# Optimization experiments

Hardware: AMD Instinct MI355X
Metric: run time of the kernel (lower is better)

## Reference

```python
import jax, jax.numpy as jnp
import numpy as np

B = 64
BAND = 16384
N_OSC = 32
CH = 64
T_IN = 32
N_NOISE_FRAMES = BAND // 4          # 4096
NOISE_STEP = BAND // N_NOISE_FRAMES  # 4 samples per noise frame
NOISE_COEFFS = NOISE_STEP // 2 + 1   # 3 rfft coefficients
N_UP = int(np.log2(N_NOISE_FRAMES) - np.log2(T_IN))  # 7 doubling blocks
LOWEST_FREQ = 20.0 / 11025.0


def _conv1d(x, w, b, pad):
    # x: (B, Cin, T), w: (Cout, Cin, K)
    out = jax.lax.conv_general_dilated(x, w, (1,), [(pad, pad)],
                                       dimension_numbers=('NCH', 'OIH', 'NCH'))
    return out + b[None, :, None]


def _leaky(x):
    return jnp.where(x > 0, x, 0.2 * x)


def _lin_interp(x, size):
    # torch F.interpolate(mode='linear', align_corners=False) along last axis
    n = x.shape[-1]
    coords = (jnp.arange(size, dtype=jnp.float32) + 0.5) * (n / size) - 0.5
    coords = jnp.clip(coords, 0.0, n - 1.0)
    lo = jnp.floor(coords).astype(jnp.int32)
    hi = jnp.minimum(lo + 1, n - 1)
    frac = (coords - lo.astype(jnp.float32)).astype(x.dtype)
    return x[..., lo] * (1.0 - frac) + x[..., hi] * frac


def setup_inputs() -> dict:
    key = jax.random.key(0)
    ks = jax.random.split(key, 16)
    s = 0.1
    return {
        'x': jax.random.normal(ks[0], (B, T_IN, CH), jnp.float32),
        'noise': jax.random.uniform(ks[1], (B, N_NOISE_FRAMES, NOISE_STEP), jnp.float32, -1.0, 1.0),
        'net_w': jax.random.normal(ks[2], (4, CH, CH, 3), jnp.float32) * s,
        'net_b': jax.random.normal(ks[3], (4, CH), jnp.float32) * s,
        'final_w': jax.random.normal(ks[4], (CH, CH, 3), jnp.float32) * s,
        'final_b': jax.random.normal(ks[5], (CH,), jnp.float32) * s,
        'amp_w': jax.random.normal(ks[6], (N_OSC, CH), jnp.float32) * s,
        'amp_b': jax.random.normal(ks[7], (N_OSC,), jnp.float32) * s,
        'freq_w': jax.random.normal(ks[8], (N_OSC, CH), jnp.float32) * s,
        'freq_b': jax.random.normal(ks[9], (N_OSC,), jnp.float32) * s,
        'nz_init_w': jax.random.normal(ks[10], (CH, CH), jnp.float32) * s,
        'nz_init_b': jax.random.normal(ks[11], (CH,), jnp.float32) * s,
        'nz_up_w': jax.random.normal(ks[12], (N_UP, CH, CH, 3), jnp.float32) * s,
        'nz_up_b': jax.random.normal(ks[13], (N_UP, CH), jnp.float32) * s,
        'nz_final_w': jax.random.normal(ks[14], (NOISE_COEFFS, CH), jnp.float32) * s,
        'nz_final_b': jax.random.normal(ks[15], (NOISE_COEFFS,), jnp.float32) * s,
    }


def reference(x, noise, net_w, net_b, final_w, final_b, amp_w, amp_b, freq_w, freq_b,
              nz_init_w, nz_init_b, nz_up_w, nz_up_b, nz_final_w, nz_final_b):
    z = jnp.transpose(x, (0, 2, 1))  # (B, CH, T_IN)
    for i in range(4):
        z = _leaky(_conv1d(z, net_w[i], net_b[i], 1))
    z = _conv1d(z, final_w, final_b, 1)

    # --- OscillatorBank: sigmoid freq (constrained), abs amp, linear upsample,
    # phase accumulation via cumsum, summed sinusoids ---
    amp = jnp.abs(jnp.einsum('bct,oc->bot', z, amp_w) + amp_b[None, :, None])
    freq = jax.nn.sigmoid(jnp.einsum('bct,oc->bot', z, freq_w) + freq_b[None, :, None])
    freq = LOWEST_FREQ + freq * (1.0 - LOWEST_FREQ)
    amp = _lin_interp(amp, BAND)    # (B, N_OSC, BAND)
    freq = _lin_interp(freq, BAND)  # (B, N_OSC, BAND)
    phase = jnp.cumsum(freq * jnp.pi, axis=-1)
    harm = jnp.sum(amp * jnp.sin(phase), axis=1, keepdims=True)  # (B, 1, BAND)

    # 1x1 conv to rfft coeffs, squared, applied per-frame to uniform noise ---
    y = jnp.einsum('bct,oc->bot', z, nz_init_w) + nz_init_b[None, :, None]
    for i in range(N_UP):
        y = jnp.repeat(y, 2, axis=-1)
        y = _leaky(_conv1d(y, nz_up_w[i], nz_up_b[i], 1))
    coeffs = jnp.einsum('bct,oc->bot', y, nz_final_w) + nz_final_b[None, :, None]
    coeffs = coeffs ** 2                      # squared=True, activation=identity
    coeffs = jnp.transpose(coeffs, (0, 2, 1))  # (B, frames, NOISE_COEFFS)
    spec = jnp.fft.rfft(noise, axis=-1, norm='ortho')   # (B, frames, NOISE_COEFFS)
    filt = spec * coeffs.astype(spec.dtype)
    nz = jnp.fft.irfft(filt, n=NOISE_STEP, axis=-1, norm='ortho')  # (B, frames, step)
    nz = nz.reshape(B, 1, BAND)

    return harm + nz
```

## Files before the change

### kernel.cpp

```cpp
#include <hip/hip_runtime.h>
#include <math.h>

#define LOWEST_FREQ_F 0.00181405895691609977f

typedef short bf16x8 __attribute__((ext_vector_type(8)));
typedef float f32x16 __attribute__((ext_vector_type(16)));

__device__ __forceinline__ float lrelu(float x) { return x > 0.f ? x : 0.2f * x; }
__device__ __forceinline__ float sin_rev(float fr) { return __builtin_amdgcn_sinf(fr); }
__device__ __forceinline__ float bf2f(unsigned short u) {
  union { unsigned int i; float f; } x; x.i = ((unsigned int)u) << 16; return x.f;
}
__device__ __forceinline__ unsigned short f2bf(float f) {
  union { float f; unsigned int i; } x; x.f = f;
  unsigned int r = x.i + 0x7FFFu + ((x.i >> 16) & 1u);
  return (unsigned short)(r >> 16);
}
__device__ __forceinline__ unsigned int pack2(float a, float b) {
  return (unsigned int)f2bf(a) | ((unsigned int)f2bf(b) << 16);
}

__global__ __launch_bounds__(256) void prep_kernel(
    const float* __restrict__ net_w, const float* __restrict__ fin_w,
    const float* __restrict__ amp_w, const float* __restrict__ frq_w,
    const float* __restrict__ nzi_w, const float* __restrict__ nzu_w,
    float* __restrict__ wtF4, float* __restrict__ awfwT,
    float* __restrict__ nzT, short* __restrict__ wfold)
{
  int idx = blockIdx.x * 256 + threadIdx.x;
  if (idx < 20480) {
    int l = idx >> 12, r = idx & 4095;
    int ci = r >> 6, co = r & 63;
    const float* src = (l < 4) ? (net_w + l * 12288) : fin_w;
    const float* wb = src + co * 192 + ci * 3;
    float4 v = make_float4(wb[0], wb[1], wb[2], 0.f);
    ((float4*)wtF4)[idx] = v;
  } else if (idx < 24576) {
    int r = idx - 20480;
    int c2 = r >> 7, rem = r & 127, o = rem >> 2, k = rem & 3;
    int c = c2 * 2 + (k >> 1);
    awfwT[r] = (k & 1) ? frq_w[o * 64 + c] : amp_w[o * 64 + c];
  } else if (idx < 28672) {
    int r = idx - 24576; int c = r >> 6, o = r & 63;
    nzT[r] = nzi_w[o * 64 + c];
  } else if (idx < 28672 + 114688) {
    int r = idx - 28672;
    int l = r >> 14, q = r & 16383;
    int pd = q >> 12, co = (q >> 6) & 63, ci = q & 63;
    const float* wb = nzu_w + l * 12288 + co * 192 + ci * 3;
    float v;
    if      (pd == 0) v = wb[0];
    else if (pd == 1) v = wb[1] + wb[2];
    else if (pd == 2) v = wb[0] + wb[1];
    else              v = wb[2];
    wfold[r] = (short)f2bf(v);
  }
}

template<int TIN>
__device__ __forceinline__ void noise_layer(
    const short* tin, short* tout, const short* __restrict__ wf,
    const float* __restrict__ bias, int tid)
{
  const int L  = tid & 63;
  const int w  = tid >> 6;
  const int mt = w & 1;
  const int ng = w >> 1;

  bf16x8 Af[4][4];
  {
    const short* wb = wf + (mt*32 + (L & 31))*64 + ((L >> 5) << 3);
    #pragma unroll
    for (int pd = 0; pd < 4; ++pd)
      #pragma unroll
      for (int ks = 0; ks < 4; ++ks)
        Af[pd][ks] = *(const bf16x8*)(wb + pd*4096 + ks*16);
  }
  f32x16 binit;
  #pragma unroll
  for (int r = 0; r < 16; ++r)
    binit[r] = bias[mt*32 + (r & 3) + 8*(r >> 2) + 4*(L >> 5)];

  if (tid < 64) { tout[tid] = 0; tout[(2*TIN + 1)*72 + tid] = 0; }

  constexpr int TOT = TIN / 32;
  constexpr int NPG = (TOT + 3) / 4;
  #pragma unroll
  for (int nt = 0; nt < NPG; ++nt) {
    int ntile = ng*NPG + nt;
    if (ntile < TOT) {
      int s = ntile*32 + (L & 31);
      const short* bp = tin + s*72 + ((L >> 5) << 3);
      f32x16 Ce = binit, Co = binit;
      #pragma unroll
      for (int ks = 0; ks < 4; ++ks) {
        bf16x8 Bm = *(const bf16x8*)(bp + ks*16);
        bf16x8 B0 = *(const bf16x8*)(bp + 72 + ks*16);
        bf16x8 Bp = *(const bf16x8*)(bp + 144 + ks*16);
        Ce = __builtin_amdgcn_mfma_f32_32x32x16_bf16(Af[0][ks], Bm, Ce, 0, 0, 0);
        Ce = __builtin_amdgcn_mfma_f32_32x32x16_bf16(Af[1][ks], B0, Ce, 0, 0, 0);
        Co = __builtin_amdgcn_mfma_f32_32x32x16_bf16(Af[2][ks], B0, Co, 0, 0, 0);
        Co = __builtin_amdgcn_mfma_f32_32x32x16_bf16(Af[3][ks], Bp, Co, 0, 0, 0);
      }
      #pragma unroll
      for (int q4 = 0; q4 < 4; ++q4) {
        int co0 = mt*32 + 8*q4 + 4*(L >> 5);
        uint2 ve, vo;
        ve.x = pack2(lrelu(Ce[4*q4+0]), lrelu(Ce[4*q4+1]));
        ve.y = pack2(lrelu(Ce[4*q4+2]), lrelu(Ce[4*q4+3]));
        vo.x = pack2(lrelu(Co[4*q4+0]), lrelu(Co[4*q4+1]));
        vo.y = pack2(lrelu(Co[4*q4+2]), lrelu(Co[4*q4+3]));
        *(uint2*)&tout[(2*s + 1)*72 + co0] = ve;
        *(uint2*)&tout[(2*s + 2)*72 + co0] = vo;
      }
    }
  }
  __syncthreads();
}

__global__ __launch_bounds__(512) void z_front(
    const float* __restrict__ x, const float* __restrict__ wtF4,
    const float* __restrict__ net_b, const float* __restrict__ fin_b,
    const float* __restrict__ awfwT, const float* __restrict__ amp_b,
    const float* __restrict__ frq_b,
    const float* __restrict__ nzT, const float* __restrict__ nzi_b,
    const short* __restrict__ wfold, const float* __restrict__ nzu_b,
    unsigned short* __restrict__ y3, float* __restrict__ amp_o,
    float* __restrict__ frq_o, float* __restrict__ ph_o)
{
  __shared__ __align__(16) char arena[86976];
  short* tileB = (short*)arena;
  short* tileA = (short*)(arena + 37152);
  float* za    = (float*)(arena + 55872);
  float* zb    = (float*)(arena + 65088);
  float* zt    = (float*)(arena + 74304);
  float* fl    = (float*)(arena + 82752);

  const int b   = blockIdx.x;
  const int tid = threadIdx.x;
  const int co  = tid & 63;
  const int wv  = tid >> 6;

  for (int idx = tid; idx < 2048; idx += 512) {
    int t = idx >> 6, c = idx & 63;
    za[c*36 + t + 1] = x[b*2048 + idx];
  }
  if (tid < 64) {
    za[tid*36] = 0.f; za[tid*36 + 33] = 0.f;
    zb[tid*36] = 0.f; zb[tid*36 + 33] = 0.f;
  }
  __syncthreads();

  float* pa = za;
  float* pb = zb;
  for (int l = 0; l < 5; ++l) {
    if (tid < 256) {
      const int q = tid >> 6;
      float bv = (l < 4) ? net_b[l*64 + co] : fin_b[co];
      float acc[8];
      #pragma unroll
      for (int j = 0; j < 8; ++j) acc[j] = bv;

      const float4* wp = ((const float4*)wtF4) + l*4096 + co;
      float4 wA[4], wB[4];
      #pragma unroll
      for (int k = 0; k < 4; ++k) wA[k] = wp[k*64];

      #pragma unroll 2
      for (int cc = 0; cc < 8; ++cc) {
        #pragma unroll
        for (int k = 0; k < 4; ++k) wB[k] = wp[(cc*8 + 4 + k)*64];
        #pragma unroll
        for (int k = 0; k < 4; ++k) {
          const int ci = cc*8 + k;
          const float* rowp = pa + ci*36 + (q << 3);
          float4 zA = *(const float4*)(rowp);
          float4 zB = *(const float4*)(rowp + 4);
          float2 zC = *(const float2*)(rowp + 8);
          float rr[10] = {zA.x, zA.y, zA.z, zA.w, zB.x, zB.y, zB.z, zB.w,
                          zC.x, zC.y};
          float4 wgt = wA[k];
          #pragma unroll
          for (int j = 0; j < 8; ++j) {
            acc[j] = fmaf(wgt.x, rr[j],   acc[j]);
            acc[j] = fmaf(wgt.y, rr[j+1], acc[j]);
            acc[j] = fmaf(wgt.z, rr[j+2], acc[j]);
          }
        }
        if (cc < 7) {
          #pragma unroll
          for (int k = 0; k < 4; ++k) wA[k] = wp[((cc+1)*8 + k)*64];
        }
        #pragma unroll
        for (int k = 0; k < 4; ++k) {
          const int ci = cc*8 + 4 + k;
          const float* rowp = pa + ci*36 + (q << 3);
          float4 zA = *(const float4*)(rowp);
          float4 zB = *(const float4*)(rowp + 4);
          float2 zC = *(const float2*)(rowp + 8);
          float rr[10] = {zA.x, zA.y, zA.z, zA.w, zB.x, zB.y, zB.z, zB.w,
                          zC.x, zC.y};
          float4 wgt = wB[k];
          #pragma unroll
          for (int j = 0; j < 8; ++j) {
            acc[j] = fmaf(wgt.x, rr[j],   acc[j]);
            acc[j] = fmaf(wgt.y, rr[j+1], acc[j]);
            acc[j] = fmaf(wgt.z, rr[j+2], acc[j]);
          }
        }
      }

      if (l < 4) {
        #pragma unroll
        for (int j = 0; j < 8; ++j)
          pb[co*36 + (q << 3) + j + 1] = lrelu(acc[j]);
      } else {
        #pragma unroll
        for (int j = 0; j < 8; ++j) {
          int t = (q << 3) + j;
          pb[co*36 + t] = acc[j];
          zt[t*66 + co] = acc[j];
        }
      }
    }
    __syncthreads();
    float* tp = pa; pa = pb; pb = tp;
  }
  const float* zf = pa;

  {
    const int q = wv;
    float bv0 = nzi_b[co];
    float acc[4];
    #pragma unroll
    for (int j = 0; j < 4; ++j) acc[j] = bv0;
    #pragma unroll 8
    for (int c = 0; c < 64; ++c) {
      float4 zv = *(const float4*)(zf + c*36 + (q << 2));
      float wvv = nzT[c*64 + co];
      acc[0] = fmaf(wvv, zv.x, acc[0]);
      acc[1] = fmaf(wvv, zv.y, acc[1]);
      acc[2] = fmaf(wvv, zv.z, acc[2]);
      acc[3] = fmaf(wvv, zv.w, acc[3]);
    }
    #pragma unroll
    for (int j = 0; j < 4; ++j)
      tileA[((q << 2) + j + 1)*72 + co] = (short)f2bf(acc[j]);
  }
  if (tid < 64) { tileA[tid] = 0; tileA[33*72 + tid] = 0; }

  #pragma unroll
  for (int tt = 0; tt < 2; ++tt) {
    int task = tid + 512*tt;
    int o = task & 31, t = task >> 5;
    float aa = amp_b[o], ff = frq_b[o];
    #pragma unroll 8
    for (int c2 = 0; c2 < 32; ++c2) {
      float4 w4 = ((const float4*)awfwT)[c2*32 + o];
      float2 zv = *(const float2*)(zt + t*66 + c2*2);
      aa = fmaf(w4.x, zv.x, aa); ff = fmaf(w4.y, zv.x, ff);
      aa = fmaf(w4.z, zv.y, aa); ff = fmaf(w4.w, zv.y, ff);
    }
    aa = fabsf(aa);
    float sg = 1.f / (1.f + expf(-ff));
    float fq = LOWEST_FREQ_F + sg * (1.f - LOWEST_FREQ_F);
    amp_o[b*1024 + o*32 + t] = aa;
    frq_o[b*1024 + o*32 + t] = fq;
    fl[o*33 + t] = fq;
  }
  __syncthreads();

  if (wv == 7 && (tid & 63) < 32) {
    const int o = tid & 31;
    double P = 256.0 * (double)fl[o*33];
    double hd = P * 0.5;
    ph_o[b*1024 + o*32] = (float)(hd - floor(hd));
    for (int i = 1; i < 32; ++i) {
      P += 256.0 * ((double)fl[o*33 + i - 1] + (double)fl[o*33 + i]);
      hd = P * 0.5;
      ph_o[b*1024 + o*32 + i] = (float)(hd - floor(hd));
    }
  }

  noise_layer<32> (tileA, tileB, wfold + 0*16384, nzu_b + 0*64, tid);
  noise_layer<64> (tileB, tileA, wfold + 1*16384, nzu_b + 1*64, tid);
  noise_layer<128>(tileA, tileB, wfold + 2*16384, nzu_b + 2*64, tid);

  unsigned short* yb = y3 + (size_t)b * 16384;
  for (int c = tid; c < 2048; c += 512) {
    int row = c >> 3, pos = (c & 7) << 3;
    *(bf16x8*)(yb + c*8) = *(const bf16x8*)&tileB[(row + 1)*72 + pos];
  }
}

template<int STILE>
__global__ __launch_bounds__(256) void mfma_up_t(
    const unsigned short* __restrict__ in, unsigned short* __restrict__ out,
    const short* __restrict__ wf, const float* __restrict__ bias, int Tin)
{
  constexpr int ROWS = STILE + 2;
  constexpr int G    = STILE / 64;
  __shared__ __align__(16) short lB[ROWS * 72];

  const int b   = blockIdx.y;
  const int s0  = blockIdx.x * STILE;
  const int tid = threadIdx.x;
  const int L   = tid & 63;
  const int w   = tid >> 6;
  const int mt  = w & 1;
  const int ng  = w >> 1;

  bf16x8 Af[4][4];
  {
    const short* wb = wf + (mt*32 + (L & 31))*64 + ((L >> 5) << 3);
    #pragma unroll
    for (int pd = 0; pd < 4; ++pd)
      #pragma unroll
      for (int ks = 0; ks < 4; ++ks)
        Af[pd][ks] = *(const bf16x8*)(wb + pd*4096 + ks*16);
  }

  const unsigned short* inb = in + (size_t)b * Tin * 64;
  for (int c = tid; c < ROWS*8; c += 256) {
    int row = c >> 3, pos = (c & 7) << 3;
    int g = s0 - 1 + row;
    bf16x8 v = {0,0,0,0,0,0,0,0};
    if (g >= 0 && g < Tin) v = *(const bf16x8*)(inb + (size_t)g*64 + pos);
    *(bf16x8*)&lB[row*72 + pos] = v;
  }

  f32x16 binit;
  #pragma unroll
  for (int r = 0; r < 16; ++r)
    binit[r] = bias[mt*32 + (r & 3) + 8*(r >> 2) + 4*(L >> 5)];

  __syncthreads();

  unsigned short* outb = out + (size_t)b * (2*Tin) * 64;
  #pragma unroll
  for (int nt = 0; nt < G; ++nt) {
    int s_loc = ng*(32*G) + nt*32 + (L & 31);
    const short* bp = lB + s_loc*72 + ((L >> 5) << 3);
    f32x16 Ce = binit, Co = binit;
    #pragma unroll
    for (int ks = 0; ks < 4; ++ks) {
      bf16x8 Bm = *(const bf16x8*)(bp + ks*16);
      bf16x8 B0 = *(const bf16x8*)(bp + 72 + ks*16);
      bf16x8 Bp = *(const bf16x8*)(bp + 144 + ks*16);
      Ce = __builtin_amdgcn_mfma_f32_32x32x16_bf16(Af[0][ks], Bm, Ce, 0, 0, 0);
      Ce = __builtin_amdgcn_mfma_f32_32x32x16_bf16(Af[1][ks], B0, Ce, 0, 0, 0);
      Co = __builtin_amdgcn_mfma_f32_32x32x16_bf16(Af[2][ks], B0, Co, 0, 0, 0);
      Co = __builtin_amdgcn_mfma_f32_32x32x16_bf16(Af[3][ks], Bp, Co, 0, 0, 0);
    }
    int t0 = (s0 + s_loc) * 2;
    #pragma unroll
    for (int q4 = 0; q4 < 4; ++q4) {
      int co0 = mt*32 + 8*q4 + 4*(L >> 5);
      uint2 ve, vo;
      ve.x = pack2(lrelu(Ce[4*q4+0]), lrelu(Ce[4*q4+1]));
      ve.y = pack2(lrelu(Ce[4*q4+2]), lrelu(Ce[4*q4+3]));
      vo.x = pack2(lrelu(Co[4*q4+0]), lrelu(Co[4*q4+1]));
      vo.y = pack2(lrelu(Co[4*q4+2]), lrelu(Co[4*q4+3]));
      *(uint2*)(outb + (size_t)t0*64 + co0)     = ve;
      *(uint2*)(outb + (size_t)(t0+1)*64 + co0) = vo;
    }
  }
}

__global__ __launch_bounds__(256) void final_fused(
    const unsigned short* __restrict__ in,
    const short* __restrict__ wf, const float* __restrict__ bias,
    const float* __restrict__ nzf_w, const float* __restrict__ nzf_b,
    const float* __restrict__ noise,
    const float* __restrict__ amp, const float* __restrict__ frq,
    const float* __restrict__ ph, float* __restrict__ out)
{
  constexpr int STILE = 128, Tin = 2048, ROWS = STILE + 2, G = STILE / 64;
  __shared__ __align__(16) short lB[ROWS * 72];
  __shared__ __align__(16) short yT[256 * 72];
  __shared__ float al[1024], fqv[1024], pl[1024];
  __shared__ float wl[192];

  const int b   = blockIdx.y;
  const int s0  = blockIdx.x * STILE;
  const int tid = threadIdx.x;
  const int L   = tid & 63;
  const int w   = tid >> 6;
  const int mt  = w & 1;
  const int ng  = w >> 1;

  for (int i = tid; i < 1024; i += 256) {
    al[i]  = amp[b*1024 + i];
    fqv[i] = frq[b*1024 + i];
    pl[i]  = ph[b*1024 + i];
  }
  if (tid < 192) { int o = tid >> 6, c = tid & 63; wl[c*3 + o] = nzf_w[tid]; }

  bf16x8 Af[4][4];
  {
    const short* wb = wf + (mt*32 + (L & 31))*64 + ((L >> 5) << 3);
    #pragma unroll
    for (int pd = 0; pd < 4; ++pd)
      #pragma unroll
      for (int ks = 0; ks < 4; ++ks)
        Af[pd][ks] = *(const bf16x8*)(wb + pd*4096 + ks*16);
  }

  const unsigned short* inb = in + (size_t)b * Tin * 64;
  for (int c = tid; c < ROWS*8; c += 256) {
    int row = c >> 3, pos = (c & 7) << 3;
    int g = s0 - 1 + row;
    bf16x8 v = {0,0,0,0,0,0,0,0};
    if (g >= 0 && g < Tin) v = *(const bf16x8*)(inb + (size_t)g*64 + pos);
    *(bf16x8*)&lB[row*72 + pos] = v;
  }

  f32x16 binit;
  #pragma unroll
  for (int r = 0; r < 16; ++r)
    binit[r] = bias[mt*32 + (r & 3) + 8*(r >> 2) + 4*(L >> 5)];

  __syncthreads();

  #pragma unroll
  for (int nt = 0; nt < G; ++nt) {
    int s_loc = ng*(32*G) + nt*32 + (L & 31);
    const short* bp = lB + s_loc*72 + ((L >> 5) << 3);
    f32x16 Ce = binit, Co = binit;
    #pragma unroll
    for (int ks = 0; ks < 4; ++ks) {
      bf16x8 Bm = *(const bf16x8*)(bp + ks*16);
      bf16x8 B0 = *(const bf16x8*)(bp + 72 + ks*16);
      bf16x8 Bp = *(const bf16x8*)(bp + 144 + ks*16);
      Ce = __builtin_amdgcn_mfma_f32_32x32x16_bf16(Af[0][ks], Bm, Ce, 0, 0, 0);
      Ce = __builtin_amdgcn_mfma_f32_32x32x16_bf16(Af[1][ks], B0, Ce, 0, 0, 0);
      Co = __builtin_amdgcn_mfma_f32_32x32x16_bf16(Af[2][ks], B0, Co, 0, 0, 0);
      Co = __builtin_amdgcn_mfma_f32_32x32x16_bf16(Af[3][ks], Bp, Co, 0, 0, 0);
    }
    #pragma unroll
    for (int q4 = 0; q4 < 4; ++q4) {
      int co0 = mt*32 + 8*q4 + 4*(L >> 5);
      uint2 ve, vo;
      ve.x = pack2(lrelu(Ce[4*q4+0]), lrelu(Ce[4*q4+1]));
      ve.y = pack2(lrelu(Ce[4*q4+2]), lrelu(Ce[4*q4+3]));
      vo.x = pack2(lrelu(Co[4*q4+0]), lrelu(Co[4*q4+1]));
      vo.y = pack2(lrelu(Co[4*q4+2]), lrelu(Co[4*q4+3]));
      *(uint2*)&yT[(2*s_loc)*72 + co0]     = ve;
      *(uint2*)&yT[(2*s_loc + 1)*72 + co0] = vo;
    }
  }
  __syncthreads();

  {
    const short* yr = &yT[tid * 72];
    float c0 = nzf_b[0], c1 = nzf_b[1], c2 = nzf_b[2];
    #pragma unroll
    for (int c8 = 0; c8 < 8; ++c8) {
      bf16x8 v = *(const bf16x8*)(yr + c8*8);
      #pragma unroll
      for (int j = 0; j < 8; ++j) {
        float yv = bf2f((unsigned short)v[j]);
        int c = c8*8 + j;
        c0 = fmaf(wl[c*3+0], yv, c0);
        c1 = fmaf(wl[c*3+1], yv, c1);
        c2 = fmaf(wl[c*3+2], yv, c2);
      }
    }
    c0 *= c0; c1 *= c1; c2 *= c2;

    const int fb = 2*s0 + tid;
    const float4 n = *(const float4*)(noise + ((size_t)b*4096 + fb)*4);
    float F0  = c0 * (n.x + n.y + n.z + n.w) * 0.5f;
    float F1r = c1 * (n.x - n.z) * 0.5f;
    float F1i = -(c1 * (n.y - n.w) * 0.5f);
    float F2  = c2 * (n.x - n.y + n.z - n.w) * 0.5f;
    float r0 = 0.5f * (F0 + 2.f*F1r + F2);
    float r1 = 0.5f * (F0 - 2.f*F1i - F2);
    float r2 = 0.5f * (F0 - 2.f*F1r + F2);
    float r3 = 0.5f * (F0 + 2.f*F1i - F2);

    const int t0 = fb * 4;
    float s0a = 0.f, s1a = 0.f, s2a = 0.f, s3a = 0.f;
    if (t0 < 256) {
      const float tp = (float)(t0 + 1) * 0.5f;
      #pragma unroll 4
      for (int o = 0; o < 32; ++o) {
        float f0 = fqv[o*32], am = al[o*32];
        float hf = 0.5f * f0;
        float v0 = tp * f0, v1 = v0 + hf, v2 = v1 + hf, v3 = v2 + hf;
        s0a += am * sin_rev(v0 - floorf(v0));
        s1a += am * sin_rev(v1 - floorf(v1));
        s2a += am * sin_rev(v2 - floorf(v2));
        s3a += am * sin_rev(v3 - floorf(v3));
      }
    } else if (t0 >= 16128) {
      const float tp = (float)(t0 - 16127) * 0.5f;
      #pragma unroll 4
      for (int o = 0; o < 32; ++o) {
        float f0 = fqv[o*32 + 31], am = al[o*32 + 31], p = pl[o*32 + 31];
        float hf = 0.5f * f0;
        float v0 = p + tp * f0, v1 = v0 + hf, v2 = v1 + hf, v3 = v2 + hf;
        s0a += am * sin_rev(v0 - floorf(v0));
        s1a += am * sin_rev(v1 - floorf(v1));
        s2a += am * sin_rev(v2 - floorf(v2));
        s3a += am * sin_rev(v3 - floorf(v3));
      }
    } else {
      const int i  = (t0 - 256) >> 9;
      const int m0 = (t0 - 256) & 511;
      float mm[4], fa[4], mq[4];
      #pragma unroll
      for (int js = 0; js < 4; ++js) {
        float mmv = (float)(m0 + 1 + js);
        mm[js] = mmv;
        fa[js] = ((float)(m0 + js) + 0.5f) * (1.f/512.f);
        mq[js] = mmv * mmv * (1.f/1024.f);
      }
      #pragma unroll 4
      for (int o = 0; o < 32; ++o) {
        float f0 = fqv[o*32 + i], f1 = fqv[o*32 + i + 1];
        float a0 = al[o*32 + i],  a1 = al[o*32 + i + 1];
        float p  = pl[o*32 + i];
        float df = f1 - f0, da = a1 - a0;
        #pragma unroll
        for (int js = 0; js < 4; ++js) {
          float av   = fmaf(da, fa[js], a0);
          float part = fmaf(df, mq[js], mm[js] * f0);
          float v    = fmaf(part, 0.5f, p);
          float fr   = v - floorf(v);
          float sv   = av * sin_rev(fr);
          if      (js == 0) s0a += sv;
          else if (js == 1) s1a += sv;
          else if (js == 2) s2a += sv;
          else              s3a += sv;
        }
      }
    }
    float4 res = make_float4(s0a + r0, s1a + r1, s2a + r2, s3a + r3);
    *(float4*)(out + ((size_t)b*4096 + fb)*4) = res;
  }
}

extern "C" void kernel_launch(void* const* d_in, const int* in_sizes, int n_in,
                              void* d_out, int out_size, void* d_ws, size_t ws_size,
                              hipStream_t stream) {
  (void)in_sizes; (void)n_in; (void)out_size; (void)ws_size;
  const float* x     = (const float*)d_in[0];
  const float* noise = (const float*)d_in[1];
  const float* net_w = (const float*)d_in[2];
  const float* net_b = (const float*)d_in[3];
  const float* fin_w = (const float*)d_in[4];
  const float* fin_b = (const float*)d_in[5];
  const float* amp_w = (const float*)d_in[6];
  const float* amp_b = (const float*)d_in[7];
  const float* frq_w = (const float*)d_in[8];
  const float* frq_b = (const float*)d_in[9];
  const float* nzi_w = (const float*)d_in[10];
  const float* nzi_b = (const float*)d_in[11];
  const float* nzu_w = (const float*)d_in[12];
  const float* nzu_b = (const float*)d_in[13];
  const float* nzf_w = (const float*)d_in[14];
  const float* nzf_b = (const float*)d_in[15];
  float* out = (float*)d_out;

  short* y3    = (short*)d_ws;
  short* y4    = y3 + (size_t)64*256*64;
  short* y5    = y4 + (size_t)64*512*64;
  short* y6    = y5 + (size_t)64*1024*64;
  short* wfold = y6 + (size_t)64*2048*64;
  float* wtF4  = (float*)(wfold + 7*16384);
  float* awfwT = wtF4 + 81920;
  float* nzT   = awfwT + 4096;
  float* ampv  = nzT + 4096;
  float* frqv  = ampv + 65536;
  float* phv   = frqv + 65536;

  prep_kernel<<<dim3(560), dim3(256), 0, stream>>>(
      net_w, fin_w, amp_w, frq_w, nzi_w, nzu_w, wtF4, awfwT, nzT, wfold);

  z_front<<<dim3(64), dim3(512), 0, stream>>>(
      x, wtF4, net_b, fin_b, awfwT, amp_b, frq_b, nzT, nzi_b,
      wfold, nzu_b, (unsigned short*)y3, ampv, frqv, phv);

  mfma_up_t<64> <<<dim3(4, 64), dim3(256), 0, stream>>>(
      (unsigned short*)y3, (unsigned short*)y4, wfold + 3*16384, nzu_b + 3*64, 256);
  mfma_up_t<128><<<dim3(4, 64), dim3(256), 0, stream>>>(
      (unsigned short*)y4, (unsigned short*)y5, wfold + 4*16384, nzu_b + 4*64, 512);
  mfma_up_t<128><<<dim3(8, 64), dim3(256), 0, stream>>>(
      (unsigned short*)y5, (unsigned short*)y6, wfold + 5*16384, nzu_b + 5*64, 1024);

  final_fused<<<dim3(16, 64), dim3(256), 0, stream>>>(
      (unsigned short*)y6, wfold + 6*16384, nzu_b + 6*64,
      nzf_w, nzf_b, noise, ampv, frqv, phv, out);
}
```

Measured before the change: 210.9 us.

## Fuse three noise upsample layers into one kernel with halo recompute

```diff
diff --git a/kernel.cpp b/kernel.cpp
--- a/kernel.cpp
+++ b/kernel.cpp
@@ -118,6 +118,113 @@
   __syncthreads();
 }
 
+template<int NT, int ROFF, bool TOGLOBAL>
+__device__ __forceinline__ void up_stage(
+    const short* bin, short* bout, unsigned short* gout,
+    const short* __restrict__ wf, const float* __restrict__ bias, int tid)
+{
+  const int L  = tid & 63;
+  const int w  = tid >> 6;
+  const int mt = w & 1;
+  const int pg = w >> 1;
+
+  bf16x8 Af[4][4];
+  {
+    const short* wb = wf + (mt*32 + (L & 31))*64 + ((L >> 5) << 3);
+    #pragma unroll
+    for (int pd = 0; pd < 4; ++pd)
+      #pragma unroll
+      for (int ks = 0; ks < 4; ++ks)
+        Af[pd][ks] = *(const bf16x8*)(wb + pd*4096 + ks*16);
+  }
+  f32x16 binit;
+  #pragma unroll
+  for (int r = 0; r < 16; ++r)
+    binit[r] = bias[mt*32 + (r & 3) + 8*(r >> 2) + 4*(L >> 5)];
+
+  for (int n = pg; n < NT; n += 2) {
+    int sl = n*32 + (L & 31);
+    const short* bp = bin + (sl + ROFF)*72 + ((L >> 5) << 3);
+    f32x16 Ce = binit, Co = binit;
+    #pragma unroll
+    for (int ks = 0; ks < 4; ++ks) {
+      bf16x8 Bm = *(const bf16x8*)(bp + ks*16);
+      bf16x8 B0 = *(const bf16x8*)(bp + 72 + ks*16);
+      bf16x8 Bp = *(const bf16x8*)(bp + 144 + ks*16);
+      Ce = __builtin_amdgcn_mfma_f32_32x32x16_bf16(Af[0][ks], Bm, Ce, 0, 0, 0);
+      Ce = __builtin_amdgcn_mfma_f32_32x32x16_bf16(Af[1][ks], B0, Ce, 0, 0, 0);
+      Co = __builtin_amdgcn_mfma_f32_32x32x16_bf16(Af[2][ks], B0, Co, 0, 0, 0);
+      Co = __builtin_amdgcn_mfma_f32_32x32x16_bf16(Af[3][ks], Bp, Co, 0, 0, 0);
+    }
+    #pragma unroll
+    for (int q4 = 0; q4 < 4; ++q4) {
+      int co0 = mt*32 + 8*q4 + 4*(L >> 5);
+      uint2 ve, vo;
+      ve.x = pack2(lrelu(Ce[4*q4+0]), lrelu(Ce[4*q4+1]));
+      ve.y = pack2(lrelu(Ce[4*q4+2]), lrelu(Ce[4*q4+3]));
+      vo.x = pack2(lrelu(Co[4*q4+0]), lrelu(Co[4*q4+1]));
+      vo.y = pack2(lrelu(Co[4*q4+2]), lrelu(Co[4*q4+3]));
+      if (TOGLOBAL) {
+        *(uint2*)(gout + (size_t)(2*sl)*64 + co0)     = ve;
+        *(uint2*)(gout + (size_t)(2*sl + 1)*64 + co0) = vo;
+      } else {
+        *(uint2*)&bout[(2*sl)*72 + co0]     = ve;
+        *(uint2*)&bout[(2*sl + 1)*72 + co0] = vo;
+      }
+    }
+  }
+}
+
+__global__ __launch_bounds__(256) void up345(
+    const unsigned short* __restrict__ y3, unsigned short* __restrict__ y6,
+    const short* __restrict__ wfold, const float* __restrict__ nzu_b)
+{
+  __shared__ __align__(16) short s3[66*72];
+  __shared__ __align__(16) short s4[128*72];
+  __shared__ __align__(16) short s5[192*72];
+
+  const int b   = blockIdx.y;
+  const int bx  = blockIdx.x;
+  const int tid = threadIdx.x;
+
+  const unsigned short* inb = y3 + (size_t)b * 256 * 64;
+  for (int c = tid; c < 66*8; c += 256) {
+    int row = c >> 3, pos = (c & 7) << 3;
+    int g = 32*bx - 2 + row;
+    bf16x8 v = {0,0,0,0,0,0,0,0};
+    if (g >= 0 && g < 256) v = *(const bf16x8*)(inb + (size_t)g*64 + pos);
+    *(bf16x8*)&s3[row*72 + pos] = v;
+  }
+  __syncthreads();
+
+  up_stage<2,0,false>(s3, s4, nullptr, wfold + 3*16384, nzu_b + 3*64, tid);
+  __syncthreads();
+  if (bx == 0) {
+    if (tid < 128) s4[(tid >> 6)*72 + (tid & 63)] = 0;
+  } else if (bx == 7) {
+    for (int i = tid; i < 62*64; i += 256) {
+      int r = 66 + (i >> 6);
+      s4[r*72 + (i & 63)] = 0;
+    }
+  }
+  __syncthreads();
+
+  up_stage<3,0,false>(s4, s5, nullptr, wfold + 4*16384, nzu_b + 4*64, tid);
+  __syncthreads();
+  if (bx == 0) {
+    if (tid < 128) s5[(tid >> 6)*72 + (tid & 63)] = 0;
+  } else if (bx == 7) {
+    for (int i = tid; i < 62*64; i += 256) {
+      int r = 130 + (i >> 6);
+      s5[r*72 + (i & 63)] = 0;
+    }
+  }
+  __syncthreads();
+
+  unsigned short* outb = y6 + ((size_t)b*2048 + 256*bx) * 64;
+  up_stage<4,1,true>(s5, nullptr, outb, wfold + 5*16384, nzu_b + 5*64, tid);
+}
+
 __global__ __launch_bounds__(512) void z_front(
     const float* __restrict__ x, const float* __restrict__ wtF4,
     const float* __restrict__ net_b, const float* __restrict__ fin_b,
@@ -154,34 +261,33 @@
   float* pa = za;
   float* pb = zb;
   for (int l = 0; l < 5; ++l) {
-    if (tid < 256) {
-      const int q = tid >> 6;
+    {
+      const int t0 = wv << 2;
       float bv = (l < 4) ? net_b[l*64 + co] : fin_b[co];
-      float acc[8];
-      #pragma unroll
-      for (int j = 0; j < 8; ++j) acc[j] = bv;
+      float acc[4];
+      #pragma unroll
+      for (int j = 0; j < 4; ++j) acc[j] = bv;
 
       const float4* wp = ((const float4*)wtF4) + l*4096 + co;
-      float4 wA[4], wB[4];
-      #pragma unroll
-      for (int k = 0; k < 4; ++k) wA[k] = wp[k*64];
-
-      #pragma unroll 2
+      float4 wCur[8], wNxt[8];
+      #pragma unroll
+      for (int k = 0; k < 8; ++k) wCur[k] = wp[k*64];
+
       for (int cc = 0; cc < 8; ++cc) {
+        if (cc < 7) {
+          #pragma unroll
+          for (int k = 0; k < 8; ++k) wNxt[k] = wp[((cc+1)*8 + k)*64];
+        }
         #pragma unroll
-        for (int k = 0; k < 4; ++k) wB[k] = wp[(cc*8 + 4 + k)*64];
-        #pragma unroll
-        for (int k = 0; k < 4; ++k) {
+        for (int k = 0; k < 8; ++k) {
           const int ci = cc*8 + k;
-          const float* rowp = pa + ci*36 + (q << 3);
+          const float* rowp = pa + ci*36 + t0;
           float4 zA = *(const float4*)(rowp);
-          float4 zB = *(const float4*)(rowp + 4);
-          float2 zC = *(const float2*)(rowp + 8);
-          float rr[10] = {zA.x, zA.y, zA.z, zA.w, zB.x, zB.y, zB.z, zB.w,
-                          zC.x, zC.y};
-          float4 wgt = wA[k];
+          float2 zB = *(const float2*)(rowp + 4);
+          float rr[6] = {zA.x, zA.y, zA.z, zA.w, zB.x, zB.y};
+          float4 wgt = wCur[k];
           #pragma unroll
-          for (int j = 0; j < 8; ++j) {
+          for (int j = 0; j < 4; ++j) {
             acc[j] = fmaf(wgt.x, rr[j],   acc[j]);
             acc[j] = fmaf(wgt.y, rr[j+1], acc[j]);
             acc[j] = fmaf(wgt.z, rr[j+2], acc[j]);
@@ -189,35 +295,18 @@
         }
         if (cc < 7) {
           #pragma unroll
-          for (int k = 0; k < 4; ++k) wA[k] = wp[((cc+1)*8 + k)*64];
-        }
-        #pragma unroll
-        for (int k = 0; k < 4; ++k) {
-          const int ci = cc*8 + 4 + k;
-          const float* rowp = pa + ci*36 + (q << 3);
-          float4 zA = *(const float4*)(rowp);
-          float4 zB = *(const float4*)(rowp + 4);
-          float2 zC = *(const float2*)(rowp + 8);
-          float rr[10] = {zA.x, zA.y, zA.z, zA.w, zB.x, zB.y, zB.z, zB.w,
-                          zC.x, zC.y};
-          float4 wgt = wB[k];
-          #pragma unroll
-          for (int j = 0; j < 8; ++j) {
-            acc[j] = fmaf(wgt.x, rr[j],   acc[j]);
-            acc[j] = fmaf(wgt.y, rr[j+1], acc[j]);
-            acc[j] = fmaf(wgt.z, rr[j+2], acc[j]);
-          }
+          for (int k = 0; k < 8; ++k) wCur[k] = wNxt[k];
         }
       }
 
       if (l < 4) {
         #pragma unroll
-        for (int j = 0; j < 8; ++j)
-          pb[co*36 + (q << 3) + j + 1] = lrelu(acc[j]);
+        for (int j = 0; j < 4; ++j)
+          pb[co*36 + t0 + j + 1] = lrelu(acc[j]);
       } else {
         #pragma unroll
-        for (int j = 0; j < 8; ++j) {
-          int t = (q << 3) + j;
+        for (int j = 0; j < 4; ++j) {
+          int t = t0 + j;
           pb[co*36 + t] = acc[j];
           zt[t*66 + co] = acc[j];
         }
@@ -290,80 +379,6 @@
   for (int c = tid; c < 2048; c += 512) {
     int row = c >> 3, pos = (c & 7) << 3;
     *(bf16x8*)(yb + c*8) = *(const bf16x8*)&tileB[(row + 1)*72 + pos];
-  }
-}
-
-template<int STILE>
-__global__ __launch_bounds__(256) void mfma_up_t(
-    const unsigned short* __restrict__ in, unsigned short* __restrict__ out,
-    const short* __restrict__ wf, const float* __restrict__ bias, int Tin)
-{
-  constexpr int ROWS = STILE + 2;
-  constexpr int G    = STILE / 64;
-  __shared__ __align__(16) short lB[ROWS * 72];
-
-  const int b   = blockIdx.y;
-  const int s0  = blockIdx.x * STILE;
-  const int tid = threadIdx.x;
-  const int L   = tid & 63;
-  const int w   = tid >> 6;
-  const int mt  = w & 1;
-  const int ng  = w >> 1;
-
-  bf16x8 Af[4][4];
-  {
-    const short* wb = wf + (mt*32 + (L & 31))*64 + ((L >> 5) << 3);
-    #pragma unroll
-    for (int pd = 0; pd < 4; ++pd)
-      #pragma unroll
-      for (int ks = 0; ks < 4; ++ks)
-        Af[pd][ks] = *(const bf16x8*)(wb + pd*4096 + ks*16);
-  }
-
-  const unsigned short* inb = in + (size_t)b * Tin * 64;
-  for (int c = tid; c < ROWS*8; c += 256) {
-    int row = c >> 3, pos = (c & 7) << 3;
-    int g = s0 - 1 + row;
-    bf16x8 v = {0,0,0,0,0,0,0,0};
-    if (g >= 0 && g < Tin) v = *(const bf16x8*)(inb + (size_t)g*64 + pos);
-    *(bf16x8*)&lB[row*72 + pos] = v;
-  }
-
-  f32x16 binit;
-  #pragma unroll
-  for (int r = 0; r < 16; ++r)
-    binit[r] = bias[mt*32 + (r & 3) + 8*(r >> 2) + 4*(L >> 5)];
-
-  __syncthreads();
-
-  unsigned short* outb = out + (size_t)b * (2*Tin) * 64;
-  #pragma unroll
-  for (int nt = 0; nt < G; ++nt) {
-    int s_loc = ng*(32*G) + nt*32 + (L & 31);
-    const short* bp = lB + s_loc*72 + ((L >> 5) << 3);
-    f32x16 Ce = binit, Co = binit;
-    #pragma unroll
-    for (int ks = 0; ks < 4; ++ks) {
-      bf16x8 Bm = *(const bf16x8*)(bp + ks*16);
-      bf16x8 B0 = *(const bf16x8*)(bp + 72 + ks*16);
-      bf16x8 Bp = *(const bf16x8*)(bp + 144 + ks*16);
-      Ce = __builtin_amdgcn_mfma_f32_32x32x16_bf16(Af[0][ks], Bm, Ce, 0, 0, 0);
-      Ce = __builtin_amdgcn_mfma_f32_32x32x16_bf16(Af[1][ks], B0, Ce, 0, 0, 0);
-      Co = __builtin_amdgcn_mfma_f32_32x32x16_bf16(Af[2][ks], B0, Co, 0, 0, 0);
-      Co = __builtin_amdgcn_mfma_f32_32x32x16_bf16(Af[3][ks], Bp, Co, 0, 0, 0);
-    }
-    int t0 = (s0 + s_loc) * 2;
-    #pragma unroll
-    for (int q4 = 0; q4 < 4; ++q4) {
-      int co0 = mt*32 + 8*q4 + 4*(L >> 5);
-      uint2 ve, vo;
-      ve.x = pack2(lrelu(Ce[4*q4+0]), lrelu(Ce[4*q4+1]));
-      ve.y = pack2(lrelu(Ce[4*q4+2]), lrelu(Ce[4*q4+3]));
-      vo.x = pack2(lrelu(Co[4*q4+0]), lrelu(Co[4*q4+1]));
-      vo.y = pack2(lrelu(Co[4*q4+2]), lrelu(Co[4*q4+3]));
-      *(uint2*)(outb + (size_t)t0*64 + co0)     = ve;
-      *(uint2*)(outb + (size_t)(t0+1)*64 + co0) = vo;
-    }
   }
 }
 
@@ -564,9 +579,7 @@
   float* out = (float*)d_out;
 
   short* y3    = (short*)d_ws;
-  short* y4    = y3 + (size_t)64*256*64;
-  short* y5    = y4 + (size_t)64*512*64;
-  short* y6    = y5 + (size_t)64*1024*64;
+  short* y6    = y3 + (size_t)64*256*64;
   short* wfold = y6 + (size_t)64*2048*64;
   float* wtF4  = (float*)(wfold + 7*16384);
   float* awfwT = wtF4 + 81920;
@@ -582,12 +595,8 @@
       x, wtF4, net_b, fin_b, awfwT, amp_b, frq_b, nzT, nzi_b,
       wfold, nzu_b, (unsigned short*)y3, ampv, frqv, phv);
 
-  mfma_up_t<64> <<<dim3(4, 64), dim3(256), 0, stream>>>(
-      (unsigned short*)y3, (unsigned short*)y4, wfold + 3*16384, nzu_b + 3*64, 256);
-  mfma_up_t<128><<<dim3(4, 64), dim3(256), 0, stream>>>(
-      (unsigned short*)y4, (unsigned short*)y5, wfold + 4*16384, nzu_b + 4*64, 512);
-  mfma_up_t<128><<<dim3(8, 64), dim3(256), 0, stream>>>(
-      (unsigned short*)y5, (unsigned short*)y6, wfold + 5*16384, nzu_b + 5*64, 1024);
+  up345<<<dim3(8, 64), dim3(256), 0, stream>>>(
+      (unsigned short*)y3, (unsigned short*)y6, wfold, nzu_b);
 
   final_fused<<<dim3(16, 64), dim3(256), 0, stream>>>(
       (unsigned short*)y6, wfold + 6*16384, nzu_b + 6*64,
```

After: 204.7 us. 1.03x faster.
